# Kernel optimization log

Measured on AMD Instinct MI355X. Metric: run time of the kernel, lower is better.

Reference implementation:

```python
import jax, jax.numpy as jnp
import numpy as np

B, T, H = 128, 512, 512  # batch, max timesteps, hidden (= input_size = output_size)


def setup_inputs() -> dict:
    key = jax.random.key(0)
    k1, k2, k3, k4 = jax.random.split(key, 4)
    x = jax.random.normal(k1, (B, T, H), dtype=jnp.float32)
    scale = 1.0 / np.sqrt(H)
    # torch.nn.Linear default init: U(-1/sqrt(fan_in), 1/sqrt(fan_in))
    W_in = jax.random.uniform(k2, (H, 6 * H), minval=-scale, maxval=scale, dtype=jnp.float32)
    b_in = jax.random.uniform(k3, (6 * H,), minval=-scale, maxval=scale, dtype=jnp.float32)
    # PackedSequence semantics: lengths sorted descending, longest == T
    lengths = jax.random.randint(k4, (B,), 1, T + 1)
    lengths = jnp.sort(lengths)[::-1].at[0].set(T).astype(jnp.int64)
    return {"x": x, "lengths": lengths, "W_in": W_in, "b_in": b_in}


def reference(x, lengths, W_in, b_in):
    # Faithful to the source: input_linearity is applied to BOTH the timestep
    # input and the previous state (the module never uses state_linearity in
    # forward). The ragged batch slicing [0:current_length_index+1] combined
    # with re-zeroing the full-batch state each step is exactly equivalent to
    # masking with (t < lengths) for sorted-descending lengths.
    Bx, Tx, _ = x.shape
    Hs = W_in.shape[0]
    proj_x = jnp.einsum('bti,io->bto', x, W_in) + b_in  # [B,T,6H], hoisted out of the loop

    def step(carry, inp):
        h, c = carry
        px, t = inp  # px: [B,6H]
        g = px + (h @ W_in + b_in)  # projected_input + projected_state
        i = jax.nn.sigmoid(g[:, 0 * Hs:1 * Hs])
        f = jax.nn.sigmoid(g[:, 1 * Hs:2 * Hs])
        m = jnp.tanh(g[:, 2 * Hs:3 * Hs])
        o = jax.nn.sigmoid(g[:, 3 * Hs:4 * Hs])
        c_new = i * m + f * c
        out = o * jnp.tanh(c_new)
        hw = jax.nn.sigmoid(g[:, 4 * Hs:5 * Hs])
        out = hw * out + (1.0 - hw) * px[:, 5 * Hs:6 * Hs]  # highway proj uses input only
        active = (t < lengths)[:, None]  # [B,1]
        h_new = jnp.where(active, out, 0.0)
        c_new = jnp.where(active, c_new, 0.0)
        return (h_new, c_new), h_new

    init = (jnp.zeros((Bx, Hs), x.dtype), jnp.zeros((Bx, Hs), x.dtype))
    _, ys = jax.lax.scan(step, init, (proj_x.transpose(1, 0, 2), jnp.arange(Tx)))
    return ys.transpose(1, 0, 2)  # [B,T,H], zero past each sequence length
```

## Files before the change

### kernel.cpp

```cpp
#include <hip/hip_runtime.h>
#include <hip/hip_bf16.h>

#define Tz 512
#define Hz 512
#define NG 8
#define BG 16
#define SL 16
#define NWAVE 6
#define NTHR (NWAVE * 64)
#define SIXH (6 * Hz)
#define HB_U32 (BG * Hz)
#define WS_U32 (2 * NG * HB_U32)

typedef __bf16 bf16x8 __attribute__((ext_vector_type(8)));
typedef float f32x4 __attribute__((ext_vector_type(4)));
typedef unsigned int u32;
typedef u32 u32x4v __attribute__((ext_vector_type(4)));

__device__ __forceinline__ u32x4v ld_coh_x4(const u32* p) {
  u32x4v r;
  asm volatile("global_load_dwordx4 %0, %1, off sc0 sc1" : "=v"(r) : "v"(p) : "memory");
  return r;
}
__device__ __forceinline__ void st_coh_u32(u32* p, u32 v) {
  asm volatile("global_store_dword %0, %1, off sc0 sc1" :: "v"(p), "v"(v) : "memory");
}
__device__ __forceinline__ void vm_wait0() {
  asm volatile("s_waitcnt vmcnt(0)" ::: "memory");
  __builtin_amdgcn_sched_barrier(0);
}
__device__ __forceinline__ void bar_lds() {
  asm volatile("s_waitcnt lgkmcnt(0)" ::: "memory");
  __builtin_amdgcn_s_barrier();
  __builtin_amdgcn_sched_barrier(0);
}
__device__ __forceinline__ float sigf(float x) { return 1.f / (1.f + __expf(-x)); }
__device__ __forceinline__ float tanh_f(float x) { return 2.f / (1.f + __expf(-2.f * x)) - 1.f; }
__device__ __forceinline__ u32 pk_bf16(float a, float b) {
  unsigned short lo = __builtin_bit_cast(unsigned short, (__bf16)a);
  unsigned short hi = __builtin_bit_cast(unsigned short, (__bf16)b);
  return (u32)lo | ((u32)hi << 16);
}

__global__ void lstm_init(u32* ws) {
  int i = blockIdx.x * blockDim.x + threadIdx.x;
  ws[i] = 0xFFFF0000u;
}

__global__ __launch_bounds__(NTHR) void lstm_main(
    const float* __restrict__ x, const int* __restrict__ lens,
    const float* __restrict__ Wg, const float* __restrict__ bg,
    float* __restrict__ out, u32* __restrict__ hb)
{
  const int tid = threadIdx.x;
  const int l   = tid & 63;
  const int w   = tid >> 6;
  const int wg  = blockIdx.x;
  const int gi  = wg & 7;
  const int si  = wg >> 3;
  const int oct = l >> 4;
  const int lm  = l & 15;

  __shared__ __align__(16) char xs[2][BG * Hz * 2];
  __shared__ __align__(16) char hs[BG * Hz * 2];
  __shared__ float gs[NWAVE][BG][SL];

  const int colg = w * Hz + si * SL + lm;
  bf16x8 wf[16];
#pragma unroll
  for (int s = 0; s < 16; ++s) {
#pragma unroll
    for (int j = 0; j < 8; ++j) {
      wf[s][j] = (__bf16)Wg[(size_t)(32 * s + 8 * oct + j) * SIXH + colg];
    }
  }
  const float bv = bg[colg];
  const float bias = (w < 5) ? 2.f * bv : bv;

  const int erow = tid >> 4;
  const int ecol = tid & 15;
  float cc = 0.f;
  int mylen = 0;
  if (tid < 256) mylen = lens[gi * BG + erow];

  float4 f[8];

  if (tid < 256) {
    const float4* xr = (const float4*)(x + ((size_t)(gi * BG + erow) * Tz + 0) * Hz + ecol * 32);
    float4 f0[8];
#pragma unroll
    for (int q = 0; q < 8; ++q) f0[q] = xr[q];
#pragma unroll
    for (int Q = 0; Q < 4; ++Q) {
      u32x4v v = { pk_bf16(f0[2*Q].x, f0[2*Q].y),   pk_bf16(f0[2*Q].z, f0[2*Q].w),
                   pk_bf16(f0[2*Q+1].x, f0[2*Q+1].y), pk_bf16(f0[2*Q+1].z, f0[2*Q+1].w) };
      int byte = (erow * 1024 + ecol * 64 + 16 * Q) ^ ((erow & 7) << 4);
      *(u32x4v*)(&xs[0][byte]) = v;
    }
    const float4* xr1 = (const float4*)(x + ((size_t)(gi * BG + erow) * Tz + 1) * Hz + ecol * 32);
#pragma unroll
    for (int q = 0; q < 8; ++q) f[q] = xr1[q];
  }
  __syncthreads();

  for (int t = 0; t < Tz; ++t) {
    const bool do_h = (t > 0) && (tid < 256);
    const u32* hp = hb + ((size_t)((t + 1) & 1) * NG + gi) * HB_U32 + erow * Hz + ecol * 32;
    u32x4v hv4[8];
    if (tid < 256 && t + 1 < Tz) {
#pragma unroll
      for (int Q = 0; Q < 4; ++Q) {
        u32x4v v = { pk_bf16(f[2*Q].x, f[2*Q].y),   pk_bf16(f[2*Q].z, f[2*Q].w),
                     pk_bf16(f[2*Q+1].x, f[2*Q+1].y), pk_bf16(f[2*Q+1].z, f[2*Q+1].w) };
        int byte = (erow * 1024 + ecol * 64 + 16 * Q) ^ ((erow & 7) << 4);
        *(u32x4v*)(&xs[(t + 1) & 1][byte]) = v;
      }
    }
    if (t > 0) {
      asm volatile("s_sleep 8" ::: "memory");
    }
    if (do_h) {
#pragma unroll
      for (int q = 0; q < 8; ++q) hv4[q] = ld_coh_x4(hp + 4 * q);
    }
    f32x4 acc0; acc0[0] = bias; acc0[1] = bias; acc0[2] = bias; acc0[3] = bias;
    f32x4 acc1; acc1[0] = 0.f; acc1[1] = 0.f; acc1[2] = 0.f; acc1[3] = 0.f;
    {
      const char* xb = xs[t & 1];
#pragma unroll
      for (int s = 0; s < 16; ++s) {
        int byte = (lm * 1024 + 64 * s + 16 * oct) ^ ((lm & 7) << 4);
        bf16x8 a = *(const bf16x8*)(xb + byte);
        if (s & 1) acc1 = __builtin_amdgcn_mfma_f32_16x16x32_bf16(a, wf[s], acc1, 0, 0, 0);
        else       acc0 = __builtin_amdgcn_mfma_f32_16x16x32_bf16(a, wf[s], acc0, 0, 0, 0);
      }
    }
    if (tid < 256) vm_wait0();
    if (do_h) {
      const u32 etag = (u32)(t - 1);
      u32 badmask = 0;
#pragma unroll
      for (int q = 0; q < 8; ++q) {
        bool b = false;
#pragma unroll
        for (int j = 0; j < 4; ++j) b |= ((hv4[q][j] >> 16) != etag);
        badmask |= (u32)b << q;
      }
      int guard = 0;
      while (__builtin_expect(badmask != 0, 0)) {
#pragma unroll
        for (int q = 0; q < 8; ++q)
          if (badmask & (1u << q)) hv4[q] = ld_coh_x4(hp + 4 * q);
        vm_wait0();
        u32 nb = 0;
#pragma unroll
        for (int q = 0; q < 8; ++q) {
          bool b = false;
#pragma unroll
          for (int j = 0; j < 4; ++j) b |= ((hv4[q][j] >> 16) != etag);
          nb |= (u32)b << q;
        }
        badmask = nb;
        if (++guard > 1000000) break;
      }
#pragma unroll
      for (int k2 = 0; k2 < 4; ++k2) {
        u32x4v o;
#pragma unroll
        for (int m = 0; m < 4; ++m) {
          int c = 8 * k2 + 2 * m;
          o[m] = __builtin_amdgcn_perm(hv4[(c + 1) >> 2][(c + 1) & 3],
                                       hv4[c >> 2][c & 3], 0x05040100u);
        }
        int byte = (erow * 1024 + ecol * 64 + 16 * k2) ^ ((erow & 7) << 4);
        *(u32x4v*)(&hs[byte]) = o;
      }
    }
    if (tid < 256 && t + 2 < Tz) {
      const float4* xr = (const float4*)(x + ((size_t)(gi * BG + erow) * Tz + (t + 2)) * Hz + ecol * 32);
#pragma unroll
      for (int q = 0; q < 8; ++q) f[q] = xr[q];
    }
    bar_lds();
    if (w < 5 && t > 0) {
#pragma unroll
      for (int s = 0; s < 16; ++s) {
        int byte = (lm * 1024 + 64 * s + 16 * oct) ^ ((lm & 7) << 4);
        bf16x8 a = *(const bf16x8*)(hs + byte);
        if (s & 1) acc1 = __builtin_amdgcn_mfma_f32_16x16x32_bf16(a, wf[s], acc1, 0, 0, 0);
        else       acc0 = __builtin_amdgcn_mfma_f32_16x16x32_bf16(a, wf[s], acc0, 0, 0, 0);
      }
    }
    {
      f32x4 g = acc0 + acc1;
#pragma unroll
      for (int r = 0; r < 4; ++r) gs[w][oct * 4 + r][lm] = g[r];
    }
    bar_lds();
    if (tid < 256) {
      float g0 = gs[0][erow][ecol], g1 = gs[1][erow][ecol], g2 = gs[2][erow][ecol];
      float g3 = gs[3][erow][ecol], g4 = gs[4][erow][ecol], px5 = gs[5][erow][ecol];
      float ig = sigf(g0), fg = sigf(g1), mg = tanh_f(g2), og = sigf(g3), hg = sigf(g4);
      float cn = ig * mg + fg * cc;
      float ot = og * tanh_f(cn);
      ot = hg * ot + (1.f - hg) * px5;
      bool act = t < mylen;
      float hv = act ? ot : 0.f;
      cc = act ? cn : 0.f;
      u32 tagged = ((u32)t << 16) | (u32)__builtin_bit_cast(unsigned short, (__bf16)hv);
      u32* hwp = hb + ((size_t)(t & 1) * NG + gi) * HB_U32 + erow * Hz + si * SL + ecol;
      st_coh_u32(hwp, tagged);
      out[((size_t)(gi * BG + erow) * Tz + t) * Hz + si * SL + ecol] = hv;
    }
  }
}

extern "C" void kernel_launch(void* const* d_in, const int* in_sizes, int n_in,
                              void* d_out, int out_size, void* d_ws, size_t ws_size,
                              hipStream_t stream) {
  const float* x  = (const float*)d_in[0];
  const int* lens = (const int*)d_in[1];
  const float* Wg = (const float*)d_in[2];
  const float* bg = (const float*)d_in[3];
  float* out = (float*)d_out;
  u32* hb = (u32*)d_ws;

  hipLaunchKernelGGL(lstm_init, dim3(WS_U32 / 256), dim3(256), 0, stream, hb);
  hipLaunchKernelGGL(lstm_main, dim3(256), dim3(NTHR), 0, stream,
                     x, lens, Wg, bg, out, hb);
}
```

Measured before the change: 1.943 ms.

## Map workgroups to XCD-local groups and exchange hidden state through L2

New measurement: 5.619 ms. 2.89x slower.

```diff
diff --git a/kernel.cpp b/kernel.cpp
--- a/kernel.cpp
+++ b/kernel.cpp
@@ -10,20 +10,35 @@
 #define NTHR (NWAVE * 64)
 #define SIXH (6 * Hz)
 #define HB_U32 (BG * Hz)
-#define WS_U32 (2 * NG * HB_U32)
+#define BUF_U32 (2 * NG * HB_U32)
+#define META_U32 272
+#define WS_NEED ((size_t)(2 * BUF_U32 + META_U32) * 4)
 
 typedef __bf16 bf16x8 __attribute__((ext_vector_type(8)));
 typedef float f32x4 __attribute__((ext_vector_type(4)));
 typedef unsigned int u32;
 typedef u32 u32x4v __attribute__((ext_vector_type(4)));
 
-__device__ __forceinline__ u32x4v ld_coh_x4(const u32* p) {
+__device__ __forceinline__ u32x4v ld_l2_x4(const u32* p) {
+  u32x4v r;
+  asm volatile("global_load_dwordx4 %0, %1, off sc0" : "=v"(r) : "v"(p) : "memory");
+  return r;
+}
+__device__ __forceinline__ void st_l2_u32(u32* p, u32 v) {
+  asm volatile("global_store_dword %0, %1, off sc0" :: "v"(p), "v"(v) : "memory");
+}
+__device__ __forceinline__ u32x4v ld_mall_x4(const u32* p) {
   u32x4v r;
   asm volatile("global_load_dwordx4 %0, %1, off sc0 sc1" : "=v"(r) : "v"(p) : "memory");
   return r;
 }
-__device__ __forceinline__ void st_coh_u32(u32* p, u32 v) {
+__device__ __forceinline__ void st_mall_u32(u32* p, u32 v) {
   asm volatile("global_store_dword %0, %1, off sc0 sc1" :: "v"(p), "v"(v) : "memory");
+}
+__device__ __forceinline__ u32x4v ld_x4(const void* p) {
+  u32x4v r;
+  asm volatile("global_load_dwordx4 %0, %1, off" : "=v"(r) : "v"(p) : "memory");
+  return r;
 }
 __device__ __forceinline__ void vm_wait0() {
   asm volatile("s_waitcnt vmcnt(0)" ::: "memory");
@@ -36,44 +51,75 @@
 }
 __device__ __forceinline__ float sigf(float x) { return 1.f / (1.f + __expf(-x)); }
 __device__ __forceinline__ float tanh_f(float x) { return 2.f / (1.f + __expf(-2.f * x)) - 1.f; }
-__device__ __forceinline__ u32 pk_bf16(float a, float b) {
+__device__ __forceinline__ float uf(u32 b) { return __builtin_bit_cast(float, b); }
+__device__ __forceinline__ u32 pk2(float a, float b) {
   unsigned short lo = __builtin_bit_cast(unsigned short, (__bf16)a);
   unsigned short hi = __builtin_bit_cast(unsigned short, (__bf16)b);
   return (u32)lo | ((u32)hi << 16);
 }
 
-__global__ void lstm_init(u32* ws) {
+__global__ void lstm_init(u32* ws, int n) {
   int i = blockIdx.x * blockDim.x + threadIdx.x;
-  ws[i] = 0xFFFF0000u;
+  if (i < n) ws[i] = (i < 2 * BUF_U32) ? 0xFFFF0000u : 0u;
 }
 
 __global__ __launch_bounds__(NTHR) void lstm_main(
     const float* __restrict__ x, const int* __restrict__ lens,
     const float* __restrict__ Wg, const float* __restrict__ bg,
-    float* __restrict__ out, u32* __restrict__ hb)
+    float* __restrict__ out, u32* __restrict__ hbF, u32* __restrict__ hbS,
+    u32* __restrict__ meta, int use_dyn)
 {
   const int tid = threadIdx.x;
   const int l   = tid & 63;
   const int w   = tid >> 6;
   const int wg  = blockIdx.x;
-  const int gi  = wg & 7;
-  const int si  = wg >> 3;
   const int oct = l >> 4;
   const int lm  = l & 15;
 
   __shared__ __align__(16) char xs[2][BG * Hz * 2];
   __shared__ __align__(16) char hs[BG * Hz * 2];
   __shared__ float gs[NWAVE][BG][SL];
+  __shared__ char pad_1cu[28672];
+  __shared__ int sh_pair;
+
+  int gi, si;
+  if (use_dyn) {
+    if (tid == 0) {
+      u32 xcd;
+      asm volatile("s_getreg_b32 %0, hwreg(HW_REG_XCC_ID)" : "=s"(xcd));
+      xcd &= 7;
+      u32* cnt   = meta;
+      u32* flags = meta + 16;
+      u32 slot = atomicAdd(&cnt[xcd], 1u);
+      int pair = -1;
+      if (slot < 32u && atomicCAS(&flags[xcd * 32 + slot], 0u, 1u) == 0u)
+        pair = (int)(xcd * 32 + slot);
+      if (pair < 0) {
+        for (int k = 0; k < 4096 && pair < 0; ++k) {
+          int idx = (wg * 37 + k) & 255;
+          if (__hip_atomic_load(&flags[idx], __ATOMIC_RELAXED, __HIP_MEMORY_SCOPE_AGENT) == 0u
+              && atomicCAS(&flags[idx], 0u, 1u) == 0u) pair = idx;
+        }
+        if (pair < 0) pair = wg & 255;
+      }
+      sh_pair = pair;
+      if (lens[0] == -2147483647) pad_1cu[0] = 1;
+    }
+    __syncthreads();
+    gi = sh_pair >> 5; si = sh_pair & 31;
+  } else {
+    gi = wg & 7; si = wg >> 3;
+    if (tid == 0 && lens[0] == -2147483647) pad_1cu[0] = 1;
+    __syncthreads();
+  }
 
   const int colg = w * Hz + si * SL + lm;
   bf16x8 wf[16];
 #pragma unroll
-  for (int s = 0; s < 16; ++s) {
-#pragma unroll
-    for (int j = 0; j < 8; ++j) {
+  for (int s = 0; s < 16; ++s)
+#pragma unroll
+    for (int j = 0; j < 8; ++j)
       wf[s][j] = (__bf16)Wg[(size_t)(32 * s + 8 * oct + j) * SIXH + colg];
-    }
-  }
   const float bv = bg[colg];
   const float bias = (w < 5) ? 2.f * bv : bv;
 
@@ -83,50 +129,64 @@
   int mylen = 0;
   if (tid < 256) mylen = lens[gi * BG + erow];
 
-  float4 f[8];
+  u32x4v f[8];
+  u32 pnd_off = 0, pnd_tag = 0;
+
+  auto stage_x = [&](const u32x4v* fx, int par) {
+#pragma unroll
+    for (int Q = 0; Q < 4; ++Q) {
+      u32x4v v = { pk2(uf(fx[2*Q][0]),   uf(fx[2*Q][1])),
+                   pk2(uf(fx[2*Q][2]),   uf(fx[2*Q][3])),
+                   pk2(uf(fx[2*Q+1][0]), uf(fx[2*Q+1][1])),
+                   pk2(uf(fx[2*Q+1][2]), uf(fx[2*Q+1][3])) };
+      int byte = (erow * 1024 + ecol * 64 + 16 * Q) ^ ((erow & 7) << 4);
+      *(u32x4v*)(&xs[par][byte]) = v;
+    }
+  };
 
   if (tid < 256) {
-    const float4* xr = (const float4*)(x + ((size_t)(gi * BG + erow) * Tz + 0) * Hz + ecol * 32);
-    float4 f0[8];
-#pragma unroll
-    for (int q = 0; q < 8; ++q) f0[q] = xr[q];
-#pragma unroll
-    for (int Q = 0; Q < 4; ++Q) {
-      u32x4v v = { pk_bf16(f0[2*Q].x, f0[2*Q].y),   pk_bf16(f0[2*Q].z, f0[2*Q].w),
-                   pk_bf16(f0[2*Q+1].x, f0[2*Q+1].y), pk_bf16(f0[2*Q+1].z, f0[2*Q+1].w) };
-      int byte = (erow * 1024 + ecol * 64 + 16 * Q) ^ ((erow & 7) << 4);
-      *(u32x4v*)(&xs[0][byte]) = v;
-    }
-    const float4* xr1 = (const float4*)(x + ((size_t)(gi * BG + erow) * Tz + 1) * Hz + ecol * 32);
-#pragma unroll
-    for (int q = 0; q < 8; ++q) f[q] = xr1[q];
+    const char* x0 = (const char*)(x + ((size_t)(gi * BG + erow) * Tz + 0) * Hz + ecol * 32);
+#pragma unroll
+    for (int q = 0; q < 8; ++q) f[q] = ld_x4(x0 + 16 * q);
+    vm_wait0();
+    stage_x(f, 0);
+    const char* x1 = (const char*)(x + ((size_t)(gi * BG + erow) * Tz + 1) * Hz + ecol * 32);
+#pragma unroll
+    for (int q = 0; q < 8; ++q) f[q] = ld_x4(x1 + 16 * q);
+    vm_wait0();
   }
   __syncthreads();
 
   for (int t = 0; t < Tz; ++t) {
+    const int parW = t & 1, parR = (t + 1) & 1;
     const bool do_h = (t > 0) && (tid < 256);
-    const u32* hp = hb + ((size_t)((t + 1) & 1) * NG + gi) * HB_U32 + erow * Hz + ecol * 32;
+    const u32 roff = (u32)(((parR * NG + gi) * HB_U32) + erow * Hz + ecol * 32);
+    const u32* hpF = hbF + roff;
+    const u32* hpS = hbS + roff;
     u32x4v hv4[8];
-    if (tid < 256 && t + 1 < Tz) {
-#pragma unroll
-      for (int Q = 0; Q < 4; ++Q) {
-        u32x4v v = { pk_bf16(f[2*Q].x, f[2*Q].y),   pk_bf16(f[2*Q].z, f[2*Q].w),
-                     pk_bf16(f[2*Q+1].x, f[2*Q+1].y), pk_bf16(f[2*Q+1].z, f[2*Q+1].w) };
-        int byte = (erow * 1024 + ecol * 64 + 16 * Q) ^ ((erow & 7) << 4);
-        *(u32x4v*)(&xs[(t + 1) & 1][byte]) = v;
-      }
+    if (tid < 256 && t + 1 < Tz) stage_x(f, parR);
+    if (tid < 256 && t + 2 < Tz) {
+      const char* xr = (const char*)(x + ((size_t)(gi * BG + erow) * Tz + (t + 2)) * Hz + ecol * 32);
+#pragma unroll
+      for (int q = 0; q < 8; ++q) f[q] = ld_x4(xr + 16 * q);
     }
     if (t > 0) {
-      asm volatile("s_sleep 8" ::: "memory");
+      if (use_dyn) asm volatile("s_sleep 2" ::: "memory");
+      else         asm volatile("s_sleep 8" ::: "memory");
     }
     if (do_h) {
-#pragma unroll
-      for (int q = 0; q < 8; ++q) hv4[q] = ld_coh_x4(hp + 4 * q);
+      if (use_dyn) {
+#pragma unroll
+        for (int q = 0; q < 8; ++q) hv4[q] = ld_l2_x4(hpF + 4 * q);
+      } else {
+#pragma unroll
+        for (int q = 0; q < 8; ++q) hv4[q] = ld_mall_x4(hpF + 4 * q);
+      }
     }
     f32x4 acc0; acc0[0] = bias; acc0[1] = bias; acc0[2] = bias; acc0[3] = bias;
     f32x4 acc1; acc1[0] = 0.f; acc1[1] = 0.f; acc1[2] = 0.f; acc1[3] = 0.f;
     {
-      const char* xb = xs[t & 1];
+      const char* xb = xs[parW];
 #pragma unroll
       for (int s = 0; s < 16; ++s) {
         int byte = (lm * 1024 + 64 * s + 16 * oct) ^ ((lm & 7) << 4);
@@ -146,11 +206,15 @@
         for (int j = 0; j < 4; ++j) b |= ((hv4[q][j] >> 16) != etag);
         badmask |= (u32)b << q;
       }
-      int guard = 0;
+      int r = 0;
       while (__builtin_expect(badmask != 0, 0)) {
+        if (r >= 2) asm volatile("s_sleep 1" ::: "memory");
 #pragma unroll
         for (int q = 0; q < 8; ++q)
-          if (badmask & (1u << q)) hv4[q] = ld_coh_x4(hp + 4 * q);
+          if (badmask & (1u << q))
+            hv4[q] = (!use_dyn) ? ld_mall_x4(hpF + 4 * q)
+                   : (r < 6)    ? ld_l2_x4(hpF + 4 * q)
+                                : ld_mall_x4(hpS + 4 * q);
         vm_wait0();
         u32 nb = 0;
 #pragma unroll
@@ -161,7 +225,7 @@
           nb |= (u32)b << q;
         }
         badmask = nb;
-        if (++guard > 1000000) break;
+        if (++r > 1000000) break;
       }
 #pragma unroll
       for (int k2 = 0; k2 < 4; ++k2) {
@@ -176,11 +240,7 @@
         *(u32x4v*)(&hs[byte]) = o;
       }
     }
-    if (tid < 256 && t + 2 < Tz) {
-      const float4* xr = (const float4*)(x + ((size_t)(gi * BG + erow) * Tz + (t + 2)) * Hz + ecol * 32);
-#pragma unroll
-      for (int q = 0; q < 8; ++q) f[q] = xr[q];
-    }
+    if (use_dyn && t > 0 && tid < 256) st_mall_u32(hbS + pnd_off, pnd_tag);
     bar_lds();
     if (w < 5 && t > 0) {
 #pragma unroll
@@ -194,7 +254,7 @@
     {
       f32x4 g = acc0 + acc1;
 #pragma unroll
-      for (int r = 0; r < 4; ++r) gs[w][oct * 4 + r][lm] = g[r];
+      for (int r2 = 0; r2 < 4; ++r2) gs[w][oct * 4 + r2][lm] = g[r2];
     }
     bar_lds();
     if (tid < 256) {
@@ -208,8 +268,13 @@
       float hv = act ? ot : 0.f;
       cc = act ? cn : 0.f;
       u32 tagged = ((u32)t << 16) | (u32)__builtin_bit_cast(unsigned short, (__bf16)hv);
-      u32* hwp = hb + ((size_t)(t & 1) * NG + gi) * HB_U32 + erow * Hz + si * SL + ecol;
-      st_coh_u32(hwp, tagged);
+      u32 woff = (u32)(((parW * NG + gi) * HB_U32) + erow * Hz + si * SL + ecol);
+      if (use_dyn) {
+        st_l2_u32(hbF + woff, tagged);
+        pnd_off = woff; pnd_tag = tagged;
+      } else {
+        st_mall_u32(hbF + woff, tagged);
+      }
       out[((size_t)(gi * BG + erow) * Tz + t) * Hz + si * SL + ecol] = hv;
     }
   }
@@ -223,9 +288,15 @@
   const float* Wg = (const float*)d_in[2];
   const float* bg = (const float*)d_in[3];
   float* out = (float*)d_out;
-  u32* hb = (u32*)d_ws;
-
-  hipLaunchKernelGGL(lstm_init, dim3(WS_U32 / 256), dim3(256), 0, stream, hb);
+
+  u32* hbF = (u32*)d_ws;
+  const int use_dyn = (ws_size >= WS_NEED) ? 1 : 0;
+  u32* hbS  = use_dyn ? (hbF + BUF_U32)     : hbF;
+  u32* meta = use_dyn ? (hbF + 2 * BUF_U32) : hbF;
+  const int nInit = use_dyn ? (2 * BUF_U32 + META_U32) : BUF_U32;
+
+  hipLaunchKernelGGL(lstm_init, dim3((nInit + 255) / 256), dim3(256), 0, stream,
+                     hbF, nInit);
   hipLaunchKernelGGL(lstm_main, dim3(256), dim3(NTHR), 0, stream,
-                     x, lens, Wg, bg, out, hb);
-}
+                     x, lens, Wg, bg, out, hbF, hbS, meta, use_dyn);
+}
```
